# Kernel optimization log

Hardware: AMD Instinct MI355X
Metric: run time of the kernel (lower is better)

The kernel has to match this reference:

```python
import jax, jax.numpy as jnp
import numpy as np

N = 100000   # nodes
E = 500000   # edges
D = 128      # node_hidden_size
ED = 128     # edge_emb_dim
L = 8        # n_message_passes
H = 4        # num_heads
V = 8192     # node_vocab_size
G = 64       # num_graphs
A = 100      # num_actions
NFLOW = 8
NPOS = 64


def setup_inputs() -> dict:
    key = jax.random.key(0)
    ks = jax.random.split(key, 24)
    rn = lambda k, shape, s: jax.random.normal(k, shape, jnp.float32) * s
    inp = {}
    # graph tensors
    inp['x'] = jax.random.randint(ks[0], (N,), 0, V)
    inp['node_type'] = jax.random.randint(ks[1], (N,), 0, 2)
    inp['batch'] = jnp.sort(jax.random.randint(ks[2], (N,), 0, G))
    inp['edge_index'] = jax.random.randint(ks[3], (2, E), 0, N)
    inp['flow'] = jax.random.randint(ks[4], (E,), 0, NFLOW)
    inp['position'] = jax.random.randint(ks[5], (E,), 0, NPOS)
    inp['block'] = jax.random.randint(ks[6], (N,), 0, 4096)
    inp['num_graphs'] = G
    # parameters
    sd = 1.0 / np.sqrt(D)
    se = 1.0 / np.sqrt(ED)
    inp['emb_table'] = rn(ks[7], (V, D), 1.0)
    inp['flow_emb'] = rn(ks[8], (NFLOW, ED), 1.0)
    inp['pos_emb'] = rn(ks[9], (NPOS, ED), 1.0)
    inp['blk_emb'] = rn(ks[10], (2, ED), 1.0)
    inp['Wq'] = rn(ks[11], (L, D, D), sd)
    inp['Wk'] = rn(ks[12], (L, D, D), sd)
    inp['Wv'] = rn(ks[13], (L, D, D), sd)
    inp['Wek'] = rn(ks[14], (L, ED, D), se)
    inp['Wev'] = rn(ks[15], (L, ED, D), se)
    inp['Wo'] = rn(ks[16], (L, D, D), sd)
    inp['Weu'] = rn(ks[17], (L, 2 * D + ED, ED), 1.0 / np.sqrt(2 * D + ED))
    inp['QW1'] = rn(ks[18], (D + ED, D), 1.0 / np.sqrt(D + ED))
    inp['Qb1'] = jnp.zeros((D,), jnp.float32)
    inp['QW2'] = rn(ks[19], (D, A), sd)
    inp['Qb2'] = jnp.zeros((A,), jnp.float32)
    return inp


def _forward(x, node_type, batch, edge_index, flow, position, block, num_graphs,
             emb_table, flow_emb, pos_emb, blk_emb,
             Wq, Wk, Wv, Wek, Wev, Wo, Weu, QW1, Qb1, QW2, Qb2):
    src, dst = edge_index[0], edge_index[1]
    feat = emb_table[x]                                        # [N, D]
    # EdgeEncoding: flow-type + position embeddings + block-crossing indicator
    crossing = (block[src] != block[dst]).astype(jnp.int32)
    e = flow_emb[flow] + pos_emb[position] + blk_emb[crossing]  # [E, ED]

    Nn, Dd = feat.shape
    dh = Dd // H
    scale = 1.0 / np.sqrt(dh)
    n_layers = Wq.shape[0]
    for l in range(n_layers):
        q = (feat @ Wq[l]).reshape(Nn, H, dh)
        k = (feat @ Wk[l]).reshape(Nn, H, dh)
        v = (feat @ Wv[l]).reshape(Nn, H, dh)
        ek = (e @ Wek[l]).reshape(-1, H, dh)
        ev = (e @ Wev[l]).reshape(-1, H, dh)
        # per-edge attention logits, softmax over edges sharing a dst node
        scores = jnp.sum(q[dst] * (k[src] + ek), axis=-1) * scale  # [E, H]
        m = jax.lax.stop_gradient(
            jax.ops.segment_max(scores, dst, num_segments=Nn))
        ex = jnp.exp(scores - m[dst])
        den = jax.ops.segment_sum(ex, dst, num_segments=Nn)
        alpha = ex / (den[dst] + 1e-16)                            # [E, H]
        msg = alpha[..., None] * (v[src] + ev)                     # [E, H, dh]
        agg = jax.ops.segment_sum(msg, dst, num_segments=Nn).reshape(Nn, Dd)
        feat_new = jax.nn.relu(feat + agg @ Wo[l])
        e = jax.nn.relu(e + jnp.concatenate([feat[src], feat[dst], e], axis=-1) @ Weu[l])
        feat = feat_new

    # scatter_mean over instruction nodes (type == 0) per graph
    maskf = (node_type == 0).astype(feat.dtype)
    ncnt = jax.ops.segment_sum(maskf, batch, num_segments=num_graphs)
    gagg = jax.ops.segment_sum(feat * maskf[:, None], batch, num_segments=num_graphs)
    gagg = gagg / jnp.maximum(ncnt, 1.0)[:, None]
    # scatter_mean of edge features per graph (edge's graph = graph of its src node)
    eb = batch[src]
    ecnt = jax.ops.segment_sum(jnp.ones((e.shape[0],), e.dtype), eb, num_segments=num_graphs)
    eagg = jax.ops.segment_sum(e, eb, num_segments=num_graphs)
    eagg = eagg / jnp.maximum(ecnt, 1.0)[:, None]

    ga = jnp.concatenate([gagg, eagg], axis=-1)                    # [G, D+ED]
    h = jax.nn.relu(ga @ QW1 + Qb1)
    logits = h @ QW2 + Qb2
    return jax.nn.log_softmax(logits, axis=-1)


def reference(x, node_type, batch, edge_index, flow, position, block, num_graphs,
              emb_table, flow_emb, pos_emb, blk_emb,
              Wq, Wk, Wv, Wek, Wev, Wo, Weu, QW1, Qb1, QW2, Qb2):
    return _forward(x, node_type, batch, edge_index, flow, position, block,
                    int(num_graphs), emb_table, flow_emb, pos_emb, blk_emb,
                    Wq, Wk, Wv, Wek, Wev, Wo, Weu, QW1, Qb1, QW2, Qb2)
```

## Files before the change

kernel.cpp:

```cpp
#include <hip/hip_runtime.h>
#include <stdint.h>

#define NN 100000
#define NE 500000
#define DD 128
#define NL 8
#define NG 64
#define NA 100
#define DET_PAIRS 65536

typedef unsigned short u16;
typedef unsigned int u32;
typedef __attribute__((ext_vector_type(8))) short short8;
typedef __attribute__((ext_vector_type(4))) float f32x4;

union U4 { uint4 v; u16 s[8]; };

__device__ __forceinline__ float b2f(u16 u){ union{u32 i; float f;} x; x.i=((u32)u)<<16; return x.f; }
__device__ __forceinline__ u16 f2b(float f){ union{float f; u32 i;} x; x.f=f; u32 b=x.i; b += 0x7fffu + ((b>>16)&1u); return (u16)(b>>16); }

__global__ void zero_k(int* __restrict__ p, int n){
  int i = blockIdx.x*256 + threadIdx.x;
  if (i < n) p[i] = 0;
}
__global__ void diag_k(u16* __restrict__ out, int n, float val){
  int i = blockIdx.x*256 + threadIdx.x;
  if (i < n) out[i] = f2b(val);
}

__global__ void detect_k(const u16* __restrict__ raw, int* __restrict__ flags){
  int i = blockIdx.x*256 + threadIdx.x;
  int ok = 0;
  if (i < DET_PAIRS){
    u16 v = raw[2*i];
    int e = (v>>7)&0xFF;
    ok = ((e >= 107 && e <= 147) || ((v & 0x7FFFu) == 0)) ? 1 : 0;
  }
  unsigned long long b = __ballot(ok);
  if ((threadIdx.x & 63) == 0) atomicAdd(&flags[2], (int)__popcll(b));
}
__global__ void flagset_k(int* __restrict__ flags){
  if (threadIdx.x==0) flags[0] = (flags[2] < DET_PAIRS/2) ? 1 : 0;
}
__global__ void tobf16_k(const void* __restrict__ in, u16* __restrict__ out, int n,
                         const int* __restrict__ flags){
  int i = blockIdx.x*256 + threadIdx.x;
  if (i >= n) return;
  if (flags[0]) out[i] = f2b(((const float*)in)[i]);
  else          out[i] = ((const u16*)in)[i];
}
__global__ void convT_k(const void* __restrict__ in, u16* __restrict__ out, int L, int K, int Nn,
                        const int* __restrict__ flags){
  int id = blockIdx.x*256 + threadIdx.x;
  int tot = L*K*Nn;
  if (id >= tot) return;
  int l = id/(K*Nn); int r = id - l*K*Nn;
  int k = r/Nn; int n = r - k*Nn;
  u16 v;
  if (flags[0]) v = f2b(((const float*)in)[id]);
  else          v = ((const u16*)in)[id];
  out[(size_t)l*K*Nn + (size_t)n*K + k] = v;
}

__global__ void featinit_k(const int* __restrict__ x, const u16* __restrict__ emb, u16* __restrict__ feat){
  int id = blockIdx.x*256 + threadIdx.x;
  if (id >= NN*16) return;
  int row = id>>4, c8 = (id&15)*8;
  int g = x[row];
  *(uint4*)(feat + (size_t)row*DD + c8) = *(const uint4*)(emb + (size_t)g*DD + c8);
}

__global__ void count_k(const int* __restrict__ dst, int* __restrict__ cnt){
  int e = blockIdx.x*256 + threadIdx.x;
  if (e < NE) atomicAdd(&cnt[dst[e]], 1);
}
__global__ void scan1_k(const int* __restrict__ cnt, int* __restrict__ excl, int* __restrict__ bsum, int n){
  __shared__ int sh[256];
  int t = threadIdx.x, g = blockIdx.x*256 + t;
  int v = (g<n) ? cnt[g] : 0;
  sh[t] = v; __syncthreads();
  for (int d=1; d<256; d<<=1){
    int xv = (t>=d) ? sh[t-d] : 0;
    __syncthreads();
    sh[t] += xv;
    __syncthreads();
  }
  if (g<n) excl[g] = sh[t]-v;
  if (t==255) bsum[blockIdx.x] = sh[255];
}
__global__ void scan2_k(int* __restrict__ bsum, int nb){
  if (threadIdx.x==0 && blockIdx.x==0){
    int a=0;
    for (int i=0;i<nb;i++){ int x=bsum[i]; bsum[i]=a; a+=x; }
  }
}
__global__ void scan3_k(const int* __restrict__ excl, const int* __restrict__ bsum,
                        int* __restrict__ offs, int* __restrict__ cursor, int n, int total){
  int g = blockIdx.x*256 + threadIdx.x;
  if (g < n){ int o = excl[g] + bsum[g>>8]; offs[g]=o; cursor[g]=o; }
  if (g==0) offs[n] = total;
}
__global__ void fill_k(const int* __restrict__ dst, int* __restrict__ cursor, int* __restrict__ perm){
  int e = blockIdx.x*256 + threadIdx.x;
  if (e < NE){ int p = atomicAdd(&cursor[dst[e]], 1); perm[p] = e; }
}
__global__ void make_sorted_k(const int* __restrict__ perm, const int* __restrict__ src,
                              const int* __restrict__ dst, int* __restrict__ srcs, int* __restrict__ dsts){
  int i = blockIdx.x*256 + threadIdx.x;
  if (i < NE){ int ed = perm[i]; srcs[i] = src[ed]; dsts[i] = dst[ed]; }
}

__global__ void edgeinit_k(const int* __restrict__ perm, const int* __restrict__ flow,
                           const int* __restrict__ pos, const int* __restrict__ blk,
                           const int* __restrict__ srcs, const int* __restrict__ dsts,
                           const int* __restrict__ batch,
                           const u16* __restrict__ flow_emb, const u16* __restrict__ pos_emb,
                           const u16* __restrict__ blk_emb,
                           u16* __restrict__ e, int* __restrict__ ebgs){
  int id = blockIdx.x*256 + threadIdx.x;
  if (id >= NE*16) return;
  int i = id>>4, c8 = (id&15)*8;
  int ed = perm[i];
  int s = srcs[i], d = dsts[i];
  int cross = (blk[s] != blk[d]) ? 1 : 0;
  U4 a,b,c,o;
  a.v = *(const uint4*)(flow_emb + (size_t)flow[ed]*DD + c8);
  b.v = *(const uint4*)(pos_emb  + (size_t)pos[ed]*DD + c8);
  c.v = *(const uint4*)(blk_emb  + (size_t)cross*DD + c8);
  #pragma unroll
  for (int j=0;j<8;j++) o.s[j] = f2b(b2f(a.s[j]) + b2f(b.s[j]) + b2f(c.s[j]));
  *(uint4*)(e + (size_t)i*DD + c8) = o.v;
  if ((id&15)==0) ebgs[i] = batch[s];
}

__global__ __launch_bounds__(256,2) void gemm_k(
    const u16* A0, const int* __restrict__ i0,
    const u16* A1, const int* __restrict__ i1,
    const u16* A2, const int* __restrict__ i2, int nchunks,
    const u16* __restrict__ Bt, int Ktot,
    const u16* res, int do_relu,
    u16* C, int M)
{
  __shared__ u16 As[128*128];
  __shared__ u16 Bs[128*128];
  int t = threadIdx.x;
  int mbase = blockIdx.x*128;
  int lane = t & 63, w = t>>6;
  int wrow = (w>>1)*64, wcol = (w&1)*64;
  f32x4 acc[4][4];
  #pragma unroll
  for (int mi=0;mi<4;mi++)
    #pragma unroll
    for (int ni=0;ni<4;ni++){ acc[mi][ni][0]=0.f; acc[mi][ni][1]=0.f; acc[mi][ni][2]=0.f; acc[mi][ni][3]=0.f; }

  int rl_w = t>>4;
  int gw = t&15;

  for (int c=0; c<nchunks; c++){
    const u16* A = (c==0)?A0:((c==1)?A1:A2);
    const int* idx = (c==0)?i0:((c==1)?i1:i2);
    #pragma unroll
    for (int i=0;i<8;i++){
      int r = rl_w + 16*i;
      int gm = mbase + r;
      uint4 av = make_uint4(0u,0u,0u,0u);
      if (gm < M){
        size_t grow = idx ? (size_t)idx[gm] : (size_t)gm;
        av = *(const uint4*)(A + grow*DD + gw*8);
      }
      *(uint4*)(As + ((size_t)i*256 + gw*16 + rl_w)*8) = av;
      uint4 bv = *(const uint4*)(Bt + (size_t)r*Ktot + c*128 + gw*8);
      *(uint4*)(Bs + ((size_t)i*256 + gw*16 + rl_w)*8) = bv;
    }
    __syncthreads();
    int l15 = lane & 15, quad = lane>>4;
    #pragma unroll
    for (int kk=0;kk<4;kk++){
      short8 af[4], bfr[4];
      #pragma unroll
      for (int mi=0;mi<4;mi++){
        int tileR = (wrow>>4) + mi;
        af[mi] = *(const short8*)(As + ((size_t)tileR*256 + kk*64 + quad*16 + l15)*8);
      }
      #pragma unroll
      for (int ni=0;ni<4;ni++){
        int tileN = (wcol>>4) + ni;
        bfr[ni] = *(const short8*)(Bs + ((size_t)tileN*256 + kk*64 + quad*16 + l15)*8);
      }
      #pragma unroll
      for (int mi=0;mi<4;mi++)
        #pragma unroll
        for (int ni=0;ni<4;ni++)
          acc[mi][ni] = __builtin_amdgcn_mfma_f32_16x16x32_bf16(af[mi], bfr[ni], acc[mi][ni], 0, 0, 0);
    }
    __syncthreads();
  }

  int l15 = lane & 15, quad = lane>>4;
  #pragma unroll
  for (int mi=0;mi<4;mi++){
    #pragma unroll
    for (int r4=0;r4<4;r4++){
      int row = wrow + mi*16 + quad*4 + r4;
      int gm = mbase + row;
      if (gm >= M) continue;
      #pragma unroll
      for (int ni=0;ni<4;ni++){
        int col = wcol + ni*16 + l15;
        float v = acc[mi][ni][r4];
        if (res) v += b2f(res[(size_t)gm*DD + col]);
        if (do_relu && v < 0.f) v = 0.f;
        C[(size_t)gm*DD + col] = f2b(v);
      }
    }
  }
}

__global__ __launch_bounds__(256,1) void scores_fused_k(
    const u16* __restrict__ E, const u16* __restrict__ WekT,
    const u16* __restrict__ q, const u16* __restrict__ k,
    const int* __restrict__ srcs, const int* __restrict__ dsts,
    float* __restrict__ sc)
{
  __shared__ u16 As[128*128];
  __shared__ u16 Bs[128*128];
  int t = threadIdx.x;
  int ebase = blockIdx.x*128;
  int lane = t & 63, w = t>>6;
  int wrow = (w>>1)*64, wcol = (w&1)*64;
  int rl_w = t>>4, gw = t&15;
  #pragma unroll
  for (int i=0;i<8;i++){
    int r = rl_w + 16*i;
    int gm = ebase + r;
    uint4 av = make_uint4(0u,0u,0u,0u);
    if (gm < NE) av = *(const uint4*)(E + (size_t)gm*DD + gw*8);
    *(uint4*)(As + ((size_t)i*256 + gw*16 + rl_w)*8) = av;
    uint4 bv = *(const uint4*)(WekT + (size_t)r*DD + gw*8);
    *(uint4*)(Bs + ((size_t)i*256 + gw*16 + rl_w)*8) = bv;
  }
  __syncthreads();
  int l15 = lane & 15, quad = lane>>4;
  f32x4 acc[4][4];
  #pragma unroll
  for (int mi=0;mi<4;mi++)
    #pragma unroll
    for (int ni=0;ni<4;ni++){ acc[mi][ni][0]=0.f; acc[mi][ni][1]=0.f; acc[mi][ni][2]=0.f; acc[mi][ni][3]=0.f; }
  #pragma unroll
  for (int kk=0;kk<4;kk++){
    short8 af[4], bfr[4];
    #pragma unroll
    for (int mi=0;mi<4;mi++)
      af[mi] = *(const short8*)(As + ((size_t)((wrow>>4)+mi)*256 + kk*64 + quad*16 + l15)*8);
    #pragma unroll
    for (int ni=0;ni<4;ni++)
      bfr[ni] = *(const short8*)(Bs + ((size_t)((wcol>>4)+ni)*256 + kk*64 + quad*16 + l15)*8);
    #pragma unroll
    for (int mi=0;mi<4;mi++)
      #pragma unroll
      for (int ni=0;ni<4;ni++)
        acc[mi][ni] = __builtin_amdgcn_mfma_f32_16x16x32_bf16(af[mi], bfr[ni], acc[mi][ni], 0, 0, 0);
  }
  __syncthreads();
  #pragma unroll
  for (int mi=0;mi<4;mi++){
    #pragma unroll
    for (int r4=0;r4<4;r4++){
      int row = wrow + mi*16 + quad*4 + r4;
      #pragma unroll
      for (int ni=0;ni<4;ni++){
        int col = wcol + ni*16 + l15;
        As[row*128 + ((((col>>3) ^ (row&15))<<3)) + (col&7)] = f2b(acc[mi][ni][r4]);
      }
    }
  }
  __syncthreads();
  const float scale = 0.17677669529663689f;
  for (int pid = t; pid < 512; pid += 256){
    int le = pid>>2, h = pid&3;
    int e = ebase + le;
    if (e >= NE) continue;
    int s = srcs[e], d = dsts[e];
    float dot = 0.f;
    #pragma unroll
    for (int j4=0;j4<4;j4++){
      int off = h*32 + j4*8;
      U4 qv, kv, ev;
      qv.v = *(const uint4*)(q + (size_t)d*DD + off);
      kv.v = *(const uint4*)(k + (size_t)s*DD + off);
      ev.v = *(const uint4*)(As + le*128 + ((((h*4+j4) ^ (le&15))<<3)));
      #pragma unroll
      for (int j=0;j<8;j++) dot += b2f(qv.s[j]) * (b2f(kv.s[j]) + b2f(ev.s[j]));
    }
    sc[(size_t)e*4 + h] = dot * scale;
  }
}

__global__ __launch_bounds__(256,2) void nodeagg_k(
    const float* __restrict__ sc, const u16* __restrict__ v,
    const u16* __restrict__ E, const int* __restrict__ srcs,
    const int* __restrict__ offs, const u16* __restrict__ WevL,
    u16* __restrict__ agg)
{
  __shared__ float sh[16*4*129];
  int t = threadIdx.x;
  int node = blockIdx.x*16 + (t>>4);
  int sub = t & 15, h = sub>>2, p4 = sub&3;
  float uh[32];
  #pragma unroll
  for (int j=0;j<32;j++) uh[j]=0.f;
  float accv[8] = {0.f,0.f,0.f,0.f,0.f,0.f,0.f,0.f};
  int beg = 0, end = 0;
  if (node < NN){ beg = offs[node]; end = offs[node+1]; }
  float m = -1e30f, den = 0.f;
  for (int i=beg;i<end;i++){
    float s = sc[(size_t)i*4 + h];
    float mn = fmaxf(m, s);
    den = den*__expf(m-mn) + __expf(s-mn);
    m = mn;
  }
  float inv = 1.0f/(den + 1e-16f);
  int offv = h*32 + p4*8;
  for (int i=beg;i<end;i++){
    float a = __expf(sc[(size_t)i*4 + h] - m)*inv;
    U4 vv; vv.v = *(const uint4*)(v + (size_t)srcs[i]*DD + offv);
    #pragma unroll
    for (int j=0;j<8;j++) accv[j] += a*b2f(vv.s[j]);
    const u16* er = E + (size_t)i*DD + p4*32;
    #pragma unroll
    for (int qq=0;qq<4;qq++){
      U4 ee; ee.v = *(const uint4*)(er + qq*8);
      #pragma unroll
      for (int j=0;j<8;j++) uh[qq*8+j] += a*b2f(ee.s[j]);
    }
  }
  int base = ((t>>4)*4 + h)*129;
  #pragma unroll
  for (int j=0;j<32;j++) sh[base + p4*32 + j] = uh[j];
  __syncthreads();
  if (node >= NN) return;
  float o8[8];
  #pragma unroll
  for (int j=0;j<8;j++) o8[j] = accv[j];
  for (int kk=0;kk<128;kk+=4){
    float u0 = sh[base+kk], u1 = sh[base+kk+1], u2 = sh[base+kk+2], u3 = sh[base+kk+3];
    U4 w0,w1,w2,w3;
    w0.v = *(const uint4*)(WevL + (size_t)kk*DD + offv);
    w1.v = *(const uint4*)(WevL + (size_t)(kk+1)*DD + offv);
    w2.v = *(const uint4*)(WevL + (size_t)(kk+2)*DD + offv);
    w3.v = *(const uint4*)(WevL + (size_t)(kk+3)*DD + offv);
    #pragma unroll
    for (int j=0;j<8;j++)
      o8[j] += u0*b2f(w0.s[j]) + u1*b2f(w1.s[j]) + u2*b2f(w2.s[j]) + u3*b2f(w3.s[j]);
  }
  U4 o;
  #pragma unroll
  for (int j=0;j<8;j++) o.s[j] = f2b(o8[j]);
  *(uint4*)(agg + (size_t)node*DD + offv) = o.v;
}

__global__ __launch_bounds__(256,2) void pool_k(
    const u16* __restrict__ feat, const int* __restrict__ gid,
    const int* __restrict__ ntype, int nrows,
    float* __restrict__ gsum_out, float* __restrict__ gcnt_out)
{
  __shared__ float ls[NG*DD];
  __shared__ float lc[NG];
  int t = threadIdx.x;
  for (int i=t; i<NG*DD; i+=256) ls[i]=0.f;
  if (t < NG) lc[t]=0.f;
  __syncthreads();
  int grp = t>>4;
  int sub = t&15;
  int rows_per_blk = (nrows + gridDim.x - 1)/gridDim.x;
  int beg = blockIdx.x*rows_per_blk;
  int end = beg + rows_per_blk; if (end > nrows) end = nrows;
  for (int r = beg+grp; r < end; r += 16){
    if (ntype && ntype[r] != 0) continue;
    int g = gid[r];
    U4 fv; fv.v = *(const uint4*)(feat + (size_t)r*DD + sub*8);
    float* dst = &ls[g*DD + sub*8];
    #pragma unroll
    for (int j=0;j<8;j++) atomicAdd(&dst[j], b2f(fv.s[j]));
    if (sub==0) atomicAdd(&lc[g], 1.f);
  }
  __syncthreads();
  for (int i=t; i<NG*DD; i+=256){
    float v = ls[i];
    if (v != 0.f) atomicAdd(&gsum_out[i], v);
  }
  if (t < NG){
    float v = lc[t];
    if (v != 0.f) atomicAdd(&gcnt_out[t], v);
  }
}

__global__ void ganorm_k(const float* __restrict__ gsum, const float* __restrict__ gcnt,
                         const float* __restrict__ esum, const float* __restrict__ ecnt,
                         float* __restrict__ ga){
  int id = blockIdx.x*256 + threadIdx.x;
  if (id >= NG*256) return;
  int g = id>>8, c = id&255;
  float v;
  if (c < 128) v = gsum[g*DD + c] / fmaxf(gcnt[g], 1.f);
  else         v = esum[g*DD + (c-128)] / fmaxf(ecnt[g], 1.f);
  ga[(size_t)g*256 + c] = v;
}

__global__ void mlp1_k(const float* __restrict__ ga, const u16* __restrict__ QW1,
                       const u16* __restrict__ Qb1, float* __restrict__ h){
  int o = blockIdx.x*256 + threadIdx.x;
  if (o >= NG*DD) return;
  int g = o>>7, j = o&127;
  float s = b2f(Qb1[j]);
  #pragma unroll 4
  for (int kq=0;kq<256;kq++) s += ga[(size_t)g*256 + kq] * b2f(QW1[(size_t)kq*DD + j]);
  h[o] = fmaxf(s, 0.f);
}

__global__ __launch_bounds__(128) void mlp2_k(const float* __restrict__ h, const u16* __restrict__ QW2,
                       const u16* __restrict__ Qb2, void* __restrict__ out, const int* __restrict__ flags){
  __shared__ float lsh[NA];
  __shared__ float red[128];
  int g = blockIdx.x, t = threadIdx.x;
  float s = -1e30f;
  if (t < NA){
    float acc = b2f(Qb2[t]);
    #pragma unroll 4
    for (int kq=0;kq<DD;kq++) acc += h[(size_t)g*DD + kq] * b2f(QW2[(size_t)kq*NA + t]);
    lsh[t] = acc; s = acc;
  }
  red[t] = s; __syncthreads();
  for (int d=64; d>0; d>>=1){ if (t<d) red[t] = fmaxf(red[t], red[t+d]); __syncthreads(); }
  float m = red[0]; __syncthreads();
  float ex = (t < NA) ? __expf(lsh[t]-m) : 0.f;
  red[t] = ex; __syncthreads();
  for (int d=64; d>0; d>>=1){ if (t<d) red[t] += red[t+d]; __syncthreads(); }
  float lse = m + __logf(red[0]);
  if (t < NA){
    float r = lsh[t]-lse;
    if (flags[0]) ((float*)out)[(size_t)g*NA + t] = r;
    else          ((u16*)out)[(size_t)g*NA + t]  = f2b(r);
  }
}

extern "C" void kernel_launch(void* const* d_in, const int* in_sizes, int n_in,
                              void* d_out, int out_size, void* d_ws, size_t ws_size,
                              hipStream_t stream) {
  (void)in_sizes; (void)n_in;
  const int* x      = (const int*)d_in[0];
  const int* ntype  = (const int*)d_in[1];
  const int* batch  = (const int*)d_in[2];
  const int* eidx   = (const int*)d_in[3];
  const int* src    = eidx;
  const int* dstp   = eidx + NE;
  const int* flow   = (const int*)d_in[4];
  const int* pos    = (const int*)d_in[5];
  const int* blk    = (const int*)d_in[6];

  char* p = (char*)d_ws;
  auto alloc = [&](size_t bytes)->char* {
    char* r = p; p += (bytes + 255) & ~(size_t)255; return r;
  };
  u16* embB  = (u16*)alloc((size_t)8192*DD*2);
  u16* flowB = (u16*)alloc(8*DD*2);
  u16* posB  = (u16*)alloc(64*DD*2);
  u16* blkB  = (u16*)alloc(2*DD*2);
  const size_t WSZb = (size_t)NL*DD*DD*2;
  u16* WevB = (u16*)alloc(WSZb);
  u16* QW1B = (u16*)alloc((size_t)256*DD*2);
  u16* Qb1B = (u16*)alloc(DD*2);
  u16* QW2B = (u16*)alloc((size_t)DD*NA*2);
  u16* Qb2B = (u16*)alloc(NA*2);
  u16* WqT  = (u16*)alloc(WSZb);
  u16* WkT  = (u16*)alloc(WSZb);
  u16* WvT  = (u16*)alloc(WSZb);
  u16* WekT = (u16*)alloc(WSZb);
  u16* WoT  = (u16*)alloc(WSZb);
  u16* WeuT = (u16*)alloc((size_t)NL*DD*384*2);
  const size_t NB = (size_t)NN*DD*2;
  u16* A  = (u16*)alloc(NB);
  u16* QB = (u16*)alloc(NB);
  u16* KB = (u16*)alloc(NB);
  const size_t EB = (size_t)NE*DD*2;
  u16* E = (u16*)alloc(EB);
  float* scores = (float*)alloc((size_t)NE*4*4);
  int* srcs   = (int*)alloc((size_t)NE*4);
  int* dsts   = (int*)alloc((size_t)NE*4);
  int* ebgs   = (int*)alloc((size_t)NE*4);
  int* cnt    = (int*)alloc((size_t)NN*4);
  int* excl   = (int*)alloc((size_t)NN*4);
  int* bsum   = (int*)alloc(1024*4);
  int* offs   = (int*)alloc((size_t)(NN+1)*4);
  int* cursor = (int*)alloc((size_t)NN*4);
  int* perm   = (int*)alloc((size_t)NE*4);
  const int POOLN = NG*DD + NG + NG*DD + NG;
  float* poolbuf = (float*)alloc((size_t)POOLN*4);
  float* gsum = poolbuf;
  float* gcnt = poolbuf + NG*DD;
  float* esum = poolbuf + NG*DD + NG;
  float* ecnt = poolbuf + NG*DD + NG + NG*DD;
  float* ga = (float*)alloc((size_t)NG*256*4);
  float* h  = (float*)alloc((size_t)NG*DD*4);
  int* flags = (int*)alloc(16);

  size_t needed = (size_t)(p - (char*)d_ws);
  if (needed > ws_size){
    diag_k<<<(out_size+255)/256,256,0,stream>>>((u16*)d_out, out_size, (float)(ws_size>>20));
    return;
  }

  zero_k<<<1,256,0,stream>>>(flags, 4);
  detect_k<<<(DET_PAIRS+255)/256,256,0,stream>>>((const u16*)d_in[8], flags);
  flagset_k<<<1,64,0,stream>>>(flags);
  auto conv = [&](int idx, u16* dst, int n){
    tobf16_k<<<(n+255)/256,256,0,stream>>>(d_in[idx], dst, n, flags);
  };
  auto convT = [&](int idx, u16* dst, int L, int K, int Nc){
    int n = L*K*Nc;
    convT_k<<<(n+255)/256,256,0,stream>>>(d_in[idx], dst, L, K, Nc, flags);
  };
  conv(8,  embB,  8192*DD);
  conv(9,  flowB, 8*DD);
  conv(10, posB,  64*DD);
  conv(11, blkB,  2*DD);
  convT(12, WqT,  NL, DD, DD);
  convT(13, WkT,  NL, DD, DD);
  convT(14, WvT,  NL, DD, DD);
  convT(15, WekT, NL, DD, DD);
  conv(16, WevB, NL*DD*DD);
  convT(17, WoT,  NL, DD, DD);
  convT(18, WeuT, NL, 384, DD);
  conv(19, QW1B, 256*DD);
  conv(20, Qb1B, DD);
  conv(21, QW2B, DD*NA);
  conv(22, Qb2B, NA);

  zero_k<<<(NN+255)/256,256,0,stream>>>(cnt, NN);
  count_k<<<(NE+255)/256,256,0,stream>>>(dstp, cnt);
  int nb = (NN+255)/256;
  scan1_k<<<nb,256,0,stream>>>(cnt, excl, bsum, NN);
  scan2_k<<<1,64,0,stream>>>(bsum, nb);
  scan3_k<<<nb,256,0,stream>>>(excl, bsum, offs, cursor, NN, NE);
  fill_k<<<(NE+255)/256,256,0,stream>>>(dstp, cursor, perm);
  make_sorted_k<<<(NE+255)/256,256,0,stream>>>(perm, src, dstp, srcs, dsts);
  featinit_k<<<(NN*16+255)/256,256,0,stream>>>(x, embB, A);
  edgeinit_k<<<(NE*16+255)/256,256,0,stream>>>(perm, flow, pos, blk, srcs, dsts, batch,
                                               flowB, posB, blkB, E, ebgs);

  dim3 gN((NN+127)/128), gE((NE+127)/128);
  for (int l=0; l<NL; l++){
    const u16* wq  = WqT  + (size_t)l*DD*DD;
    const u16* wk  = WkT  + (size_t)l*DD*DD;
    const u16* wv  = WvT  + (size_t)l*DD*DD;
    const u16* wek = WekT + (size_t)l*DD*DD;
    const u16* wo  = WoT  + (size_t)l*DD*DD;
    const u16* wevL= WevB + (size_t)l*DD*DD;
    const u16* weu = WeuT + (size_t)l*DD*384;

    gemm_k<<<gN,256,0,stream>>>(A,nullptr,nullptr,nullptr,nullptr,nullptr,1, wq,128, nullptr,0, QB, NN);
    gemm_k<<<gN,256,0,stream>>>(A,nullptr,nullptr,nullptr,nullptr,nullptr,1, wk,128, nullptr,0, KB, NN);
    scores_fused_k<<<gE,256,0,stream>>>(E, wek, QB, KB, srcs, dsts, scores);
    gemm_k<<<gN,256,0,stream>>>(A,nullptr,nullptr,nullptr,nullptr,nullptr,1, wv,128, nullptr,0, KB, NN);
    nodeagg_k<<<(NN+15)/16,256,0,stream>>>(scores, KB, E, srcs, offs, wevL, QB);
    gemm_k<<<gE,256,0,stream>>>(A,srcs, A,dsts, E,nullptr, 3, weu,384, E,1, E, NE);
    gemm_k<<<gN,256,0,stream>>>(QB,nullptr,nullptr,nullptr,nullptr,nullptr,1, wo,128, A,1, A, NN);
  }

  zero_k<<<(POOLN+255)/256,256,0,stream>>>((int*)poolbuf, POOLN);
  pool_k<<<256,256,0,stream>>>(A, batch, ntype, NN, gsum, gcnt);
  pool_k<<<256,256,0,stream>>>(E, ebgs, nullptr, NE, esum, ecnt);
  ganorm_k<<<(NG*256+255)/256,256,0,stream>>>(gsum, gcnt, esum, ecnt, ga);
  mlp1_k<<<(NG*DD+255)/256,256,0,stream>>>(ga, QW1B, Qb1B, h);
  mlp2_k<<<NG,128,0,stream>>>(h, QW2B, Qb2B, d_out, flags);
}
```

Measured before the change: 5.230 ms.

## Replace atomic-heavy pooling with per-graph bucketed segment sums

The old pooling did per-element shared-memory float atomics into a 64x128 table for every node and edge row. The new path builds a per-graph histogram, a scan and a permutation that buckets rows by graph. Each block then sums a contiguous chunk of one graph's rows in registers and issues only 128 global atomics per block. It adds several small kernel launches and an extra gather through the permutation. Separately, the scores kernel's launch bounds are raised to allow two blocks per CU.

```diff
diff --git a/kernel.cpp b/kernel.cpp
--- a/kernel.cpp
+++ b/kernel.cpp
@@ -216,7 +216,7 @@
   }
 }
 
-__global__ __launch_bounds__(256,1) void scores_fused_k(
+__global__ __launch_bounds__(256,2) void scores_fused_k(
     const u16* __restrict__ E, const u16* __restrict__ WekT,
     const u16* __restrict__ q, const u16* __restrict__ k,
     const int* __restrict__ srcs, const int* __restrict__ dsts,
@@ -359,51 +359,77 @@
   *(uint4*)(agg + (size_t)node*DD + offv) = o.v;
 }
 
-__global__ __launch_bounds__(256,2) void pool_k(
-    const u16* __restrict__ feat, const int* __restrict__ gid,
-    const int* __restrict__ ntype, int nrows,
-    float* __restrict__ gsum_out, float* __restrict__ gcnt_out)
+__global__ void hist_k(const int* __restrict__ gid, const int* __restrict__ mask, int n,
+                       int* __restrict__ hist){
+  __shared__ int lh[NG];
+  int t = threadIdx.x;
+  if (t < NG) lh[t]=0;
+  __syncthreads();
+  int i = blockIdx.x*256 + t;
+  if (i < n && (!mask || mask[i]==0)) atomicAdd(&lh[gid[i]], 1);
+  __syncthreads();
+  if (t < NG && lh[t]) atomicAdd(&hist[t], lh[t]);
+}
+__global__ void scan64_k(const int* __restrict__ hist, int* __restrict__ base, int* __restrict__ cur){
+  if (threadIdx.x==0){
+    int a=0;
+    for (int g=0; g<NG; g++){ base[g]=a; cur[g]=a; a+=hist[g]; }
+    base[NG]=a;
+  }
+}
+__global__ void fillperm_k(const int* __restrict__ gid, const int* __restrict__ mask, int n,
+                           int* __restrict__ cur, int* __restrict__ operm){
+  __shared__ int lh[NG];
+  __shared__ int lb[NG];
+  int t = threadIdx.x;
+  if (t < NG) lh[t]=0;
+  __syncthreads();
+  int i = blockIdx.x*256 + t;
+  int g=-1, r=0;
+  if (i < n && (!mask || mask[i]==0)){ g = gid[i]; r = atomicAdd(&lh[g], 1); }
+  __syncthreads();
+  if (t < NG && lh[t]) lb[t] = atomicAdd(&cur[t], lh[t]);
+  __syncthreads();
+  if (g >= 0) operm[lb[g] + r] = i;
+}
+__global__ __launch_bounds__(256,4) void poolsum_k(
+    const u16* __restrict__ feat, const int* __restrict__ operm,
+    const int* __restrict__ base, int chunks, float* __restrict__ outsum)
 {
-  __shared__ float ls[NG*DD];
-  __shared__ float lc[NG];
-  int t = threadIdx.x;
-  for (int i=t; i<NG*DD; i+=256) ls[i]=0.f;
-  if (t < NG) lc[t]=0.f;
-  __syncthreads();
-  int grp = t>>4;
-  int sub = t&15;
-  int rows_per_blk = (nrows + gridDim.x - 1)/gridDim.x;
-  int beg = blockIdx.x*rows_per_blk;
-  int end = beg + rows_per_blk; if (end > nrows) end = nrows;
-  for (int r = beg+grp; r < end; r += 16){
-    if (ntype && ntype[r] != 0) continue;
-    int g = gid[r];
+  __shared__ float sh[16*128];
+  int g = blockIdx.x / chunks, c = blockIdx.x % chunks;
+  int beg = base[g], end = base[g+1];
+  int len = end - beg;
+  int cb = beg + (int)(((long long)len*c)/chunks);
+  int ce = beg + (int)(((long long)len*(c+1))/chunks);
+  int t = threadIdx.x, grp = t>>4, sub = t&15;
+  float acc[8] = {0.f,0.f,0.f,0.f,0.f,0.f,0.f,0.f};
+  for (int i = cb+grp; i < ce; i += 16){
+    int r = operm[i];
     U4 fv; fv.v = *(const uint4*)(feat + (size_t)r*DD + sub*8);
-    float* dst = &ls[g*DD + sub*8];
-    #pragma unroll
-    for (int j=0;j<8;j++) atomicAdd(&dst[j], b2f(fv.s[j]));
-    if (sub==0) atomicAdd(&lc[g], 1.f);
-  }
-  __syncthreads();
-  for (int i=t; i<NG*DD; i+=256){
-    float v = ls[i];
-    if (v != 0.f) atomicAdd(&gsum_out[i], v);
-  }
-  if (t < NG){
-    float v = lc[t];
-    if (v != 0.f) atomicAdd(&gcnt_out[t], v);
-  }
-}
-
-__global__ void ganorm_k(const float* __restrict__ gsum, const float* __restrict__ gcnt,
-                         const float* __restrict__ esum, const float* __restrict__ ecnt,
+    #pragma unroll
+    for (int j=0;j<8;j++) acc[j] += b2f(fv.s[j]);
+  }
+  #pragma unroll
+  for (int j=0;j<8;j++) sh[grp*128 + sub*8 + j] = acc[j];
+  __syncthreads();
+  if (t < 128){
+    float s = 0.f;
+    #pragma unroll
+    for (int r=0;r<16;r++) s += sh[r*128 + t];
+    if (s != 0.f) atomicAdd(&outsum[g*DD + t], s);
+  }
+}
+
+__global__ void ganorm_k(const float* __restrict__ gsum, const int* __restrict__ ncnt,
+                         const float* __restrict__ esum, const int* __restrict__ ecnt,
                          float* __restrict__ ga){
   int id = blockIdx.x*256 + threadIdx.x;
   if (id >= NG*256) return;
   int g = id>>8, c = id&255;
   float v;
-  if (c < 128) v = gsum[g*DD + c] / fmaxf(gcnt[g], 1.f);
-  else         v = esum[g*DD + (c-128)] / fmaxf(ecnt[g], 1.f);
+  if (c < 128) v = gsum[g*DD + c] / fmaxf((float)ncnt[g], 1.f);
+  else         v = esum[g*DD + (c-128)] / fmaxf((float)ecnt[g], 1.f);
   ga[(size_t)g*256 + c] = v;
 }
 
@@ -494,12 +520,16 @@
   int* offs   = (int*)alloc((size_t)(NN+1)*4);
   int* cursor = (int*)alloc((size_t)NN*4);
   int* perm   = (int*)alloc((size_t)NE*4);
-  const int POOLN = NG*DD + NG + NG*DD + NG;
-  float* poolbuf = (float*)alloc((size_t)POOLN*4);
-  float* gsum = poolbuf;
-  float* gcnt = poolbuf + NG*DD;
-  float* esum = poolbuf + NG*DD + NG;
-  float* ecnt = poolbuf + NG*DD + NG + NG*DD;
+  int* eperm  = (int*)alloc((size_t)NE*4);
+  int* nperm  = (int*)alloc((size_t)NN*4);
+  int* ehist  = (int*)alloc(NG*4);
+  int* ebase  = (int*)alloc((NG+1)*4);
+  int* ecur   = (int*)alloc(NG*4);
+  int* nhist  = (int*)alloc(NG*4);
+  int* nbase  = (int*)alloc((NG+1)*4);
+  int* ncur   = (int*)alloc(NG*4);
+  float* gsum = (float*)alloc((size_t)NG*DD*4);
+  float* esum = (float*)alloc((size_t)NG*DD*4);
   float* ga = (float*)alloc((size_t)NG*256*4);
   float* h  = (float*)alloc((size_t)NG*DD*4);
   int* flags = (int*)alloc(16);
@@ -567,10 +597,20 @@
     gemm_k<<<gN,256,0,stream>>>(QB,nullptr,nullptr,nullptr,nullptr,nullptr,1, wo,128, A,1, A, NN);
   }
 
-  zero_k<<<(POOLN+255)/256,256,0,stream>>>((int*)poolbuf, POOLN);
-  pool_k<<<256,256,0,stream>>>(A, batch, ntype, NN, gsum, gcnt);
-  pool_k<<<256,256,0,stream>>>(E, ebgs, nullptr, NE, esum, ecnt);
-  ganorm_k<<<(NG*256+255)/256,256,0,stream>>>(gsum, gcnt, esum, ecnt, ga);
+  zero_k<<<1,256,0,stream>>>(ehist, NG);
+  zero_k<<<1,256,0,stream>>>(nhist, NG);
+  zero_k<<<(NG*DD*2+255)/256,256,0,stream>>>((int*)gsum, NG*DD);
+  zero_k<<<(NG*DD*2+255)/256,256,0,stream>>>((int*)esum, NG*DD);
+  hist_k<<<(NE+255)/256,256,0,stream>>>(ebgs, nullptr, NE, ehist);
+  hist_k<<<(NN+255)/256,256,0,stream>>>(batch, ntype, NN, nhist);
+  scan64_k<<<1,64,0,stream>>>(ehist, ebase, ecur);
+  scan64_k<<<1,64,0,stream>>>(nhist, nbase, ncur);
+  fillperm_k<<<(NE+255)/256,256,0,stream>>>(ebgs, nullptr, NE, ecur, eperm);
+  fillperm_k<<<(NN+255)/256,256,0,stream>>>(batch, ntype, NN, ncur, nperm);
+  const int ECH = 16, NCH = 4;
+  poolsum_k<<<NG*ECH,256,0,stream>>>(E, eperm, ebase, ECH, esum);
+  poolsum_k<<<NG*NCH,256,0,stream>>>(A, nperm, nbase, NCH, gsum);
+  ganorm_k<<<(NG*256+255)/256,256,0,stream>>>(gsum, nhist, esum, ehist, ga);
   mlp1_k<<<(NG*DD+255)/256,256,0,stream>>>(ga, QW1B, Qb1B, h);
   mlp2_k<<<NG,128,0,stream>>>(h, QW2B, Qb2B, d_out, flags);
 }
```

After: 4.996 ms. -4.5%, faster.
